# Optimization experiments

Hardware: AMD Instinct MI355X
Metric: run time of the kernel (lower is better)

The kernel has to match this reference:

```python
import jax, jax.numpy as jnp
import numpy as np

INV_148 = 1.0 / 1.48  # scaling to align grids with flat-top gaussian


def _trilinear_sample(grid, pts):
    # grid: [C, D, H, W]; pts: [N, 3] in (x,y,z)=(W,H,D) normalized coords, align_corners=True,
    # padding_mode='zeros' (out-of-bounds corners contribute 0). Returns [C, N].
    C, D, H, W = grid.shape
    fx = (pts[:, 0] + 1.0) * 0.5 * (W - 1)
    fy = (pts[:, 1] + 1.0) * 0.5 * (H - 1)
    fz = (pts[:, 2] + 1.0) * 0.5 * (D - 1)
    x0 = jnp.floor(fx).astype(jnp.int32)
    y0 = jnp.floor(fy).astype(jnp.int32)
    z0 = jnp.floor(fz).astype(jnp.int32)
    wx, wy, wz = fx - x0, fy - y0, fz - z0
    out = jnp.zeros((C, pts.shape[0]), dtype=grid.dtype)
    for dz in (0, 1):
        for dy in (0, 1):
            for dx in (0, 1):
                xi, yi, zi = x0 + dx, y0 + dy, z0 + dz
                w = (wx if dx else 1.0 - wx) * (wy if dy else 1.0 - wy) * (wz if dz else 1.0 - wz)
                valid = ((xi >= 0) & (xi < W) & (yi >= 0) & (yi < H) & (zi >= 0) & (zi < D))
                v = grid[:, jnp.clip(zi, 0, D - 1), jnp.clip(yi, 0, H - 1), jnp.clip(xi, 0, W - 1)]
                out = out + v * (w * valid)
    return out


def setup_inputs() -> dict:
    key = jax.random.key(0)
    ks = jax.random.split(key, 10)
    G, Fch, Dg, N, NPL, OUT = 32, 2, 64, 524288, 64, 1
    in_dim = G * Fch
    x = jax.random.uniform(ks[0], (N, 3), minval=-1.0, maxval=1.0, dtype=jnp.float32)
    grid_scales = jax.random.uniform(ks[1], (G, 3), minval=1.5, maxval=2.5, dtype=jnp.float32)
    grid_translations = jax.random.uniform(ks[2], (G, 3), minval=-1.0, maxval=1.0, dtype=jnp.float32) * (grid_scales - 1.0)
    feature_grids = jax.random.uniform(ks[3], (G, Fch, Dg, Dg, Dg), minval=-0.001, maxval=0.001, dtype=jnp.float32)
    W0 = jax.random.normal(ks[4], (NPL, in_dim), dtype=jnp.float32) * (1.0 / np.sqrt(in_dim))
    b0 = jnp.zeros((NPL,), dtype=jnp.float32)
    W1 = jax.random.normal(ks[5], (NPL, NPL), dtype=jnp.float32) * (1.0 / np.sqrt(NPL))
    b1 = jnp.zeros((NPL,), dtype=jnp.float32)
    W2 = jax.random.normal(ks[6], (OUT, NPL), dtype=jnp.float32) * (1.0 / np.sqrt(NPL))
    b2 = jnp.zeros((OUT,), dtype=jnp.float32)
    return {"x": x, "grid_scales": grid_scales, "grid_translations": grid_translations,
            "feature_grids": feature_grids, "W0": W0, "b0": b0, "W1": W1, "b1": b1, "W2": W2, "b2": b2}


def reference(x, grid_scales, grid_translations, feature_grids, W0, b0, W1, b1, W2, b2):
    G = feature_grids.shape[0]
    N = x.shape[0]
    # transform(): per-grid affine (diag scale + translation), then * 1/1.48 -> [G, N, 3]
    local = (x[None, :, :] * grid_scales[:, None, :] + grid_translations[:, None, :]) * INV_148
    # forward detaches grid coords before grid_sample
    local = jax.lax.stop_gradient(local)
    feats = jax.vmap(_trilinear_sample)(feature_grids, local)  # [G, F, N]
    h = feats.reshape(G * feats.shape[1], N).T  # [N, G*F]
    h = jax.nn.relu(h @ W0.T + b0)
    h = jax.nn.relu(h @ W1.T + b1)
    return h @ W2.T + b2  # [N, n_outputs]
```

## Files before the change

kernel.cpp:

```cpp
#include <hip/hip_runtime.h>
#include <hip/hip_fp16.h>

#define NG    32
#define DG    64
#define NPL   64
#define CPD2  16
#define NC2   4096
#define NCELL 512
#define NPAIR (NCELL * NG)
#define HPAD  16
#define BS    512
#define TV    4096
#define HS    68

#define SWZ(i) ((i) ^ (((i) >> 6) & 28))

typedef _Float16 half8 __attribute__((ext_vector_type(8)));
typedef float    floatx4 __attribute__((ext_vector_type(4)));

__device__ __forceinline__ int morton16(int cx, int cy, int cz) {
    int m = 0;
    #pragma unroll
    for (int b = 0; b < 4; ++b)
        m |= (((cx >> b) & 1) << (3 * b))
           | (((cy >> b) & 1) << (3 * b + 1))
           | (((cz >> b) & 1) << (3 * b + 2));
    return m;
}
__device__ __forceinline__ int cell_of(float px, float py, float pz) {
    int cx = min(max((int)((px + 1.0f) * (0.5f * CPD2)), 0), CPD2 - 1);
    int cy = min(max((int)((py + 1.0f) * (0.5f * CPD2)), 0), CPD2 - 1);
    int cz = min(max((int)((pz + 1.0f) * (0.5f * CPD2)), 0), CPD2 - 1);
    return morton16(cx, cy, cz);
}

__global__ __launch_bounds__(1024)
void classify_kernel(const float* __restrict__ scales,
                     const float* __restrict__ trans,
                     unsigned* __restrict__ pairs, int* __restrict__ counters)
{
    __shared__ int   sHead, sTail;
    __shared__ float sA[NG * 3], sB[NG * 3];
    const int tid  = threadIdx.x;
    const int lane = tid & 63;
    if (tid == 0) { sHead = 0; sTail = NPAIR; }
    if (tid < NG * 3) {
        const float k = (1.0f / 1.48f) * 31.5f;
        sA[tid] = scales[tid] * k;
        sB[tid] = trans[tid] * k + 31.5f;
    }
    __syncthreads();

    for (int p = tid; p < NPAIR; p += 1024) {
        int c = p >> 5, g = p & 31;
        int cx = (c & 1)        | (((c >> 3) & 1) << 1) | (((c >> 6) & 1) << 2);
        int cy = ((c >> 1) & 1) | (((c >> 4) & 1) << 1) | (((c >> 7) & 1) << 2);
        int cz = ((c >> 2) & 1) | (((c >> 5) & 1) << 1) | (((c >> 8) & 1) << 2);
        bool skip = false, fast = true;
        #pragma unroll
        for (int d = 0; d < 3; ++d) {
            float A = sA[3 * g + d], B = sB[3 * g + d];
            int  cc = (d == 0) ? cx : ((d == 1) ? cy : cz);
            float lo = fmaf((float)cc, 0.25f, -1.0f) - 1e-4f;
            float hi = lo + 0.25f + 2e-4f;
            float fmn = fmaf(lo, A, B);
            float fmx = fmaf(hi, A, B);
            skip = skip || (fmx <= -1.0f) || (fmn >= 64.0f);
            fast = fast && (fmn >= 0.0f) && (fmx <= 62.9f);
        }
        unsigned code = ((unsigned)c << 6) | ((unsigned)g << 1) | (fast ? 1u : 0u);

        unsigned long long mAct = __ballot(!skip);
        int cntA = __popcll(mAct);
        int bA = 0, bS = 0;
        if (lane == 0) {
            bA = atomicAdd(&sHead, cntA);
            bS = atomicAdd(&sTail, -(64 - cntA));
        }
        bA = __shfl(bA, 0); bS = __shfl(bS, 0);
        unsigned long long below = (1ull << lane) - 1ull;
        if (!skip) pairs[bA + __popcll(mAct & below)] = code;
        else       pairs[bS - 1 - __popcll(~mAct & below)] = code;
    }
    __syncthreads();
    if (tid == 0) counters[0] = sHead;
}

__global__ __launch_bounds__(256)
void pack_hist_kernel(const float* __restrict__ fg, uint4* __restrict__ pg,
                      int total4, int nPack,
                      const float* __restrict__ x, int N,
                      int* __restrict__ ghist)
{
    __shared__ int lh[NC2];
    if ((int)blockIdx.x < nPack) {
        int idx = blockIdx.x * 256 + threadIdx.x;
        if (idx >= total4) return;
        int g  = idx >> 16;
        int v4 = (idx & 65535) << 2;
        const float* base = fg + ((size_t)g << 19);
        float4 a = *(const float4*)(base + v4);
        float4 b = *(const float4*)(base + (1 << 18) + v4);
        uint4 o;
        __half2 h;
        h = __floats2half2_rn(a.x, b.x); o.x = *(unsigned*)&h;
        h = __floats2half2_rn(a.y, b.y); o.y = *(unsigned*)&h;
        h = __floats2half2_rn(a.z, b.z); o.z = *(unsigned*)&h;
        h = __floats2half2_rn(a.w, b.w); o.w = *(unsigned*)&h;
        pg[idx] = o;
    } else {
        int b = blockIdx.x - nPack;
        for (int i = threadIdx.x; i < NC2; i += 256) lh[i] = 0;
        __syncthreads();
        int base = b * 1024 + threadIdx.x;
        #pragma unroll
        for (int s = 0; s < 4; ++s) {
            int n = base + s * 256;
            if (n < N) atomicAdd(&lh[cell_of(x[3*n], x[3*n+1], x[3*n+2])], 1);
        }
        __syncthreads();
        for (int i = threadIdx.x; i < NC2; i += 256) {
            int c = lh[i];
            if (c) atomicAdd(&ghist[i * HPAD], c);
        }
    }
}

__global__ __launch_bounds__(1024)
void scan_kernel(const int* __restrict__ ghist, int* __restrict__ gcursor,
                 int* __restrict__ cellstart) {
    __shared__ int tsum[1024];
    int t = threadIdx.x;
    int v0 = ghist[(t * 4 + 0) * HPAD];
    int v1 = ghist[(t * 4 + 1) * HPAD];
    int v2 = ghist[(t * 4 + 2) * HPAD];
    int v3 = ghist[(t * 4 + 3) * HPAD];
    tsum[t] = v0 + v1 + v2 + v3;
    __syncthreads();
    #pragma unroll
    for (int off = 1; off < 1024; off <<= 1) {
        int u = (t >= off) ? tsum[t - off] : 0;
        __syncthreads();
        tsum[t] += u;
        __syncthreads();
    }
    int base = (t == 0) ? 0 : tsum[t - 1];
    gcursor[(t*4+0)*HPAD] = base; cellstart[t*4+0] = base; base += v0;
    gcursor[(t*4+1)*HPAD] = base; cellstart[t*4+1] = base; base += v1;
    gcursor[(t*4+2)*HPAD] = base; cellstart[t*4+2] = base; base += v2;
    gcursor[(t*4+3)*HPAD] = base; cellstart[t*4+3] = base;
    if (t == 1023) cellstart[NC2] = tsum[1023];
}

__global__ __launch_bounds__(BS)
void scatter_kernel(const float* __restrict__ x, int N,
                    int* __restrict__ gcursor, float4* __restrict__ sorted,
                    int* __restrict__ nidx) {
    __shared__ int cnt[NC2];
    __shared__ int base[NC2];
    int tid = threadIdx.x;
    for (int i = tid; i < NC2; i += BS) cnt[i] = 0;
    __syncthreads();
    int n = blockIdx.x * BS + tid;
    float px = 0.f, py = 0.f, pz = 0.f;
    int c = 0, r = 0;
    bool act = (n < N);
    if (act) {
        px = x[3*n]; py = x[3*n+1]; pz = x[3*n+2];
        c = cell_of(px, py, pz);
        r = atomicAdd(&cnt[c], 1);
    }
    __syncthreads();
    for (int i = tid; i < NC2; i += BS) {
        int cc = cnt[i];
        base[i] = cc ? atomicAdd(&gcursor[i * HPAD], cc) : 0;
    }
    __syncthreads();
    if (act) {
        int pos = base[c] + r;
        sorted[pos] = make_float4(px, py, pz, 0.0f);
        nidx[pos]   = n;
    }
}

__device__ __forceinline__ float2 h2_to_f2(unsigned u) {
    __half2 h = *reinterpret_cast<__half2*>(&u);
    return __half22float2(h);
}

template<bool FAST>
__device__ __forceinline__ unsigned sample_tile(
    const unsigned* __restrict__ tl,
    float px, float py, float pz,
    float A0, float A1, float A2, float B0, float B1, float B2,
    int ox, int oy, int oz)
{
    float fx = fmaf(px, A0, B0);
    float fy = fmaf(py, A1, B1);
    float fz = fmaf(pz, A2, B2);
    float flx = floorf(fx), fly = floorf(fy), flz = floorf(fz);
    int x0 = (int)flx, y0 = (int)fly, z0 = (int)flz;
    float wx = fx - flx, wy = fy - fly, wz = fz - flz;

    float wxa0, wxa1, wya0, wya1, wza0, wza1;
    int ix0, ix1, iy0, iy1, iz0, iz1;
    if (FAST) {
        wxa0 = 1.0f - wx; wxa1 = wx;
        wya0 = 1.0f - wy; wya1 = wy;
        wza0 = 1.0f - wz; wza1 = wz;
        ix0 = x0 - ox;            ix1 = ix0 + 1;
        iy0 = (y0 - oy) << 4;     iy1 = iy0 + 16;
        iz0 = (z0 - oz) << 8;     iz1 = iz0 + 256;
    } else {
        wxa0 = (x0 >= 0  && x0     < DG) ? (1.0f - wx) : 0.0f;
        wxa1 = (x0 >= -1 && x0 + 1 < DG) ? wx          : 0.0f;
        wya0 = (y0 >= 0  && y0     < DG) ? (1.0f - wy) : 0.0f;
        wya1 = (y0 >= -1 && y0 + 1 < DG) ? wy          : 0.0f;
        wza0 = (z0 >= 0  && z0     < DG) ? (1.0f - wz) : 0.0f;
        wza1 = (z0 >= -1 && z0 + 1 < DG) ? wz          : 0.0f;
        ix0 = min(max(x0     - ox, 0), 15);
        ix1 = min(max(x0 + 1 - ox, 0), 15);
        iy0 = (min(max(y0     - oy, 0), 15)) << 4;
        iy1 = (min(max(y0 + 1 - oy, 0), 15)) << 4;
        iz0 = (min(max(z0     - oz, 0), 15)) << 8;
        iz1 = (min(max(z0 + 1 - oz, 0), 15)) << 8;
    }
    const int m0 = (iz0 >> 6) & 28;
    const int m1 = (iz1 >> 6) & 28;

    float w00 = wya0 * wza0, w10 = wya1 * wza0;
    float w01 = wya0 * wza1, w11 = wya1 * wza1;

    float c0 = 0.0f, c1 = 0.0f;
    float2 v;
    v = h2_to_f2(tl[(iz0+iy0+ix0)^m0]); c0 = fmaf(wxa0*w00, v.x, c0); c1 = fmaf(wxa0*w00, v.y, c1);
    v = h2_to_f2(tl[(iz0+iy0+ix1)^m0]); c0 = fmaf(wxa1*w00, v.x, c0); c1 = fmaf(wxa1*w00, v.y, c1);
    v = h2_to_f2(tl[(iz0+iy1+ix0)^m0]); c0 = fmaf(wxa0*w10, v.x, c0); c1 = fmaf(wxa0*w10, v.y, c1);
    v = h2_to_f2(tl[(iz0+iy1+ix1)^m0]); c0 = fmaf(wxa1*w10, v.x, c0); c1 = fmaf(wxa1*w10, v.y, c1);
    v = h2_to_f2(tl[(iz1+iy0+ix0)^m1]); c0 = fmaf(wxa0*w01, v.x, c0); c1 = fmaf(wxa0*w01, v.y, c1);
    v = h2_to_f2(tl[(iz1+iy0+ix1)^m1]); c0 = fmaf(wxa1*w01, v.x, c0); c1 = fmaf(wxa1*w01, v.y, c1);
    v = h2_to_f2(tl[(iz1+iy1+ix0)^m1]); c0 = fmaf(wxa0*w11, v.x, c0); c1 = fmaf(wxa0*w11, v.y, c1);
    v = h2_to_f2(tl[(iz1+iy1+ix1)^m1]); c0 = fmaf(wxa1*w11, v.x, c0); c1 = fmaf(wxa1*w11, v.y, c1);

    __half2 hv = __floats2half2_rn(c0, c1);
    return *reinterpret_cast<unsigned*>(&hv);
}

__global__ __launch_bounds__(BS)
void gather2_kernel(const float4* __restrict__ sorted,
                    const int*   __restrict__ cs16,
                    const unsigned* __restrict__ pairs,
                    const int*   __restrict__ counters,
                    const float* __restrict__ scales,
                    const float* __restrict__ trans,
                    const unsigned* __restrict__ pg,
                    unsigned* __restrict__ fb, int N)
{
    __shared__ unsigned tile[TV];

    const int tid = threadIdx.x;
    const int nA  = counters[0];
    unsigned pr   = pairs[blockIdx.x];
    const int c   = pr >> 6;
    const int g   = (pr >> 1) & 31;
    const bool fastp = pr & 1;

    int s0 = cs16[c * 8];
    int e  = cs16[c * 8 + 8];

    if ((int)blockIdx.x >= nA) {
        for (int i = s0 + tid; i < e; i += BS) fb[(size_t)g * N + i] = 0u;
        return;
    }
    if (s0 >= e) return;

    int cx = (c & 1)        | (((c >> 3) & 1) << 1) | (((c >> 6) & 1) << 2);
    int cy = ((c >> 1) & 1) | (((c >> 4) & 1) << 1) | (((c >> 7) & 1) << 2);
    int cz = ((c >> 2) & 1) | (((c >> 5) & 1) << 1) | (((c >> 8) & 1) << 2);

    const float k = (1.0f / 1.48f) * 31.5f;
    float A0 = scales[3*g+0] * k, B0 = trans[3*g+0] * k + 31.5f;
    float A1 = scales[3*g+1] * k, B1 = trans[3*g+1] * k + 31.5f;
    float A2 = scales[3*g+2] * k, B2 = trans[3*g+2] * k + 31.5f;
    int ox = min(max((int)floorf(fmaf((float)cx * 0.25f - 1.0f, A0, B0)), 0), 48);
    int oy = min(max((int)floorf(fmaf((float)cy * 0.25f - 1.0f, A1, B1)), 0), 48);
    int oz = min(max((int)floorf(fmaf((float)cz * 0.25f - 1.0f, A2, B2)), 0), 48);

    float4 q0, q1, q2;
    int  i0 = s0 + tid, i1 = s0 + BS + tid, i2 = s0 + 2 * BS + tid;
    bool a0_ = (i0 < e), a1_ = (i1 < e), a2_ = (i2 < e);
    q0 = a0_ ? sorted[i0] : make_float4(0,0,0,0);
    q1 = a1_ ? sorted[i1] : make_float4(0,0,0,0);
    q2 = a2_ ? sorted[i2] : make_float4(0,0,0,0);

    const unsigned* gb = pg + ((size_t)g << 18);
    #pragma unroll
    for (int jj = 0; jj < 8; ++jj) {
        int v = tid + (jj << 9);
        tile[SWZ(v)] = gb[((oz + (v >> 8)) << 12) + ((oy + ((v >> 4) & 15)) << 6)
                          + ox + (v & 15)];
    }
    __syncthreads();

    unsigned* dst = fb + (size_t)g * N;
    if (fastp) {
        if (a0_) dst[i0] = sample_tile<true >(tile, q0.x,q0.y,q0.z, A0,A1,A2,B0,B1,B2, ox,oy,oz);
        if (a1_) dst[i1] = sample_tile<true >(tile, q1.x,q1.y,q1.z, A0,A1,A2,B0,B1,B2, ox,oy,oz);
        if (a2_) dst[i2] = sample_tile<true >(tile, q2.x,q2.y,q2.z, A0,A1,A2,B0,B1,B2, ox,oy,oz);
    } else {
        if (a0_) dst[i0] = sample_tile<false>(tile, q0.x,q0.y,q0.z, A0,A1,A2,B0,B1,B2, ox,oy,oz);
        if (a1_) dst[i1] = sample_tile<false>(tile, q1.x,q1.y,q1.z, A0,A1,A2,B0,B1,B2, ox,oy,oz);
        if (a2_) dst[i2] = sample_tile<false>(tile, q2.x,q2.y,q2.z, A0,A1,A2,B0,B1,B2, ox,oy,oz);
    }
}

#define MBS 256
__global__ __launch_bounds__(MBS)
void mlp_kernel(const unsigned* __restrict__ fb,
                const int* __restrict__ nidx,
                const float* __restrict__ W0, const float* __restrict__ b0,
                const float* __restrict__ W1, const float* __restrict__ b1,
                const float* __restrict__ W2, const float* __restrict__ b2,
                float* __restrict__ out, int N)
{
    __shared__ __align__(16) _Float16 sW0h[NPL * NPL];
    __shared__ __align__(16) _Float16 sW1h[NPL * NPL];
    __shared__ float sb0f[NPL], sb1f[NPL], sW2f[NPL];
    __shared__ __align__(16) _Float16 sH[4][NPL * HS];

    int tid = threadIdx.x;
    for (int i = tid; i < NPL * NPL; i += MBS) {
        sW0h[i] = (_Float16)W0[i];
        sW1h[i] = (_Float16)W1[i];
    }
    if (tid < NPL) { sb0f[tid] = b0[tid]; sb1f[tid] = b1[tid]; sW2f[tid] = W2[tid]; }
    __syncthreads();

    const int wave = tid >> 6;
    const int lane = tid & 63;
    const int l15  = lane & 15;
    const int kg   = lane >> 4;
    const long wbase = (long)blockIdx.x * MBS + wave * 64;
    if (wbase >= N) return;

    half8 B0f[4][2], B1f[4][2];
    float bias0[4], bias1[4], w2v[4];
    #pragma unroll
    for (int nt = 0; nt < 4; ++nt) {
        int ch = nt * 16 + l15;
        #pragma unroll
        for (int kh = 0; kh < 2; ++kh) {
            int k = kh * 32 + kg * 8;
            B0f[nt][kh] = *(const half8*)&sW0h[ch * NPL + k];
            B1f[nt][kh] = *(const half8*)&sW1h[ch * NPL + k];
        }
        bias0[nt] = sb0f[ch];
        bias1[nt] = sb1f[ch];
        w2v[nt]   = sW2f[ch];
    }

    _Float16* H = &sH[wave][0];

    floatx4 acc[4][4];
    #pragma unroll
    for (int mt = 0; mt < 4; ++mt) {
        long pt = wbase + mt * 16 + l15;
        if (pt > N - 1) pt = N - 1;
        const unsigned* p0 = fb + (size_t)(4 * kg) * N + pt;
        const unsigned* p1 = fb + (size_t)(16 + 4 * kg) * N + pt;
        uint4 t0 = make_uint4(p0[0], p0[N], p0[2*(size_t)N], p0[3*(size_t)N]);
        uint4 t1 = make_uint4(p1[0], p1[N], p1[2*(size_t)N], p1[3*(size_t)N]);
        half8 a0 = *reinterpret_cast<half8*>(&t0);
        half8 a1 = *reinterpret_cast<half8*>(&t1);
        #pragma unroll
        for (int nt = 0; nt < 4; ++nt) {
            floatx4 cc = {0.f, 0.f, 0.f, 0.f};
            cc = __builtin_amdgcn_mfma_f32_16x16x32_f16(a0, B0f[nt][0], cc, 0, 0, 0);
            cc = __builtin_amdgcn_mfma_f32_16x16x32_f16(a1, B0f[nt][1], cc, 0, 0, 0);
            acc[mt][nt] = cc;
        }
    }
    #pragma unroll
    for (int mt = 0; mt < 4; ++mt)
        #pragma unroll
        for (int nt = 0; nt < 4; ++nt) {
            int ch = nt * 16 + l15;
            #pragma unroll
            for (int r = 0; r < 4; ++r) {
                float v = fmaxf(acc[mt][nt][r] + bias0[nt], 0.0f);
                H[(mt * 16 + kg * 4 + r) * HS + ch] = (_Float16)v;
            }
        }

    floatx4 acc2[4][4];
    #pragma unroll
    for (int mt = 0; mt < 4; ++mt) {
        const _Float16* hp = &H[(mt * 16 + l15) * HS];
        half8 a0 = *(const half8*)&hp[kg * 8];
        half8 a1 = *(const half8*)&hp[32 + kg * 8];
        #pragma unroll
        for (int nt = 0; nt < 4; ++nt) {
            floatx4 cc = {0.f, 0.f, 0.f, 0.f};
            cc = __builtin_amdgcn_mfma_f32_16x16x32_f16(a0, B1f[nt][0], cc, 0, 0, 0);
            cc = __builtin_amdgcn_mfma_f32_16x16x32_f16(a1, B1f[nt][1], cc, 0, 0, 0);
            acc2[mt][nt] = cc;
        }
    }

    float p[4][4];
    #pragma unroll
    for (int mt = 0; mt < 4; ++mt)
        #pragma unroll
        for (int r = 0; r < 4; ++r) p[mt][r] = 0.0f;
    #pragma unroll
    for (int mt = 0; mt < 4; ++mt)
        #pragma unroll
        for (int nt = 0; nt < 4; ++nt)
            #pragma unroll
            for (int r = 0; r < 4; ++r) {
                float v = fmaxf(acc2[mt][nt][r] + bias1[nt], 0.0f);
                p[mt][r] = fmaf(v, w2v[nt], p[mt][r]);
            }
    #pragma unroll
    for (int mt = 0; mt < 4; ++mt)
        #pragma unroll
        for (int r = 0; r < 4; ++r) {
            float s = p[mt][r];
            s += __shfl_xor(s, 1);
            s += __shfl_xor(s, 2);
            s += __shfl_xor(s, 4);
            s += __shfl_xor(s, 8);
            p[mt][r] = s;
        }

    float* HF = (float*)H;
    float ob = b2[0];
    if (l15 == 0) {
        #pragma unroll
        for (int mt = 0; mt < 4; ++mt)
            #pragma unroll
            for (int r = 0; r < 4; ++r)
                HF[mt * 16 + kg * 4 + r] = p[mt][r] + ob;
    }
    long pos = wbase + lane;
    if (pos < N) out[nidx[pos]] = HF[lane];
}

__global__ void pack_only_kernel(const float* __restrict__ fg,
                                 uint4* __restrict__ pg, int total4) {
    int idx = blockIdx.x * blockDim.x + threadIdx.x;
    if (idx >= total4) return;
    int g  = idx >> 16;
    int v4 = (idx & 65535) << 2;
    const float* base = fg + ((size_t)g << 19);
    float4 a = *(const float4*)(base + v4);
    float4 b = *(const float4*)(base + (1 << 18) + v4);
    uint4 o;
    __half2 h;
    h = __floats2half2_rn(a.x, b.x); o.x = *(unsigned*)&h;
    h = __floats2half2_rn(a.y, b.y); o.y = *(unsigned*)&h;
    h = __floats2half2_rn(a.z, b.z); o.z = *(unsigned*)&h;
    h = __floats2half2_rn(a.w, b.w); o.w = *(unsigned*)&h;
    pg[idx] = o;
}

__global__ __launch_bounds__(256)
void fused_fallback_kernel(const float* __restrict__ x,
                           const float* __restrict__ scales,
                           const float* __restrict__ trans,
                           const __half2* __restrict__ pg,
                           const float* __restrict__ W0, const float* __restrict__ b0,
                           const float* __restrict__ W1, const float* __restrict__ b1,
                           const float* __restrict__ W2, const float* __restrict__ b2,
                           float* __restrict__ out, int N)
{
    __shared__ float sW0[NPL*NPL], sW1[NPL*NPL], sW2[NPL], sb0[NPL], sb1[NPL];
    __shared__ float sA[NG*3], sB[NG*3];
    const int tid = threadIdx.x;
    for (int i = tid; i < NPL*NPL; i += 256) { sW0[i] = W0[i]; sW1[i] = W1[i]; }
    if (tid < NPL) { sW2[tid] = W2[tid]; sb0[tid] = b0[tid]; sb1[tid] = b1[tid]; }
    if (tid < NG*3) {
        const float k = (1.0f / 1.48f) * 31.5f;
        sA[tid] = scales[tid] * k;
        sB[tid] = trans[tid] * k + 31.5f;
    }
    __syncthreads();
    int n = blockIdx.x * 256 + tid;
    if (n >= N) return;
    float px = x[3*n], py = x[3*n+1], pz = x[3*n+2];
    float feat[2*NG];
    #pragma unroll
    for (int g = 0; g < NG; ++g) {
        float fx = fmaf(px, sA[3*g+0], sB[3*g+0]);
        float fy = fmaf(py, sA[3*g+1], sB[3*g+1]);
        float fz = fmaf(pz, sA[3*g+2], sB[3*g+2]);
        float c0 = 0.f, c1 = 0.f;
        if (fx > -1.f && fx < 64.f && fy > -1.f && fy < 64.f && fz > -1.f && fz < 64.f) {
            float flx = floorf(fx), fly = floorf(fy), flz = floorf(fz);
            int x0 = (int)flx, y0 = (int)fly, z0 = (int)flz;
            float wx = fx-flx, wy = fy-fly, wz = fz-flz;
            float wxa[2], wya[2], wza[2]; int xia[2], yia[2], zia[2];
            wxa[0] = (x0 >= 0  && x0   < DG) ? (1.f-wx) : 0.f;
            wxa[1] = (x0 >= -1 && x0+1 < DG) ? wx : 0.f;
            wya[0] = (y0 >= 0  && y0   < DG) ? (1.f-wy) : 0.f;
            wya[1] = (y0 >= -1 && y0+1 < DG) ? wy : 0.f;
            wza[0] = (z0 >= 0  && z0   < DG) ? (1.f-wz) : 0.f;
            wza[1] = (z0 >= -1 && z0+1 < DG) ? wz : 0.f;
            xia[0] = min(max(x0,0),DG-1); xia[1] = min(max(x0+1,0),DG-1);
            yia[0] = min(max(y0,0),DG-1); yia[1] = min(max(y0+1,0),DG-1);
            zia[0] = min(max(z0,0),DG-1); zia[1] = min(max(z0+1,0),DG-1);
            #pragma unroll
            for (int dz = 0; dz < 2; ++dz)
                #pragma unroll
                for (int dy = 0; dy < 2; ++dy) {
                    int rowoff = (zia[dz] << 12) + (yia[dy] << 6);
                    float wyz = wya[dy] * wza[dz];
                    #pragma unroll
                    for (int dx = 0; dx < 2; ++dx) {
                        float w = wxa[dx] * wyz;
                        float2 vf = __half22float2(pg[(g << 18) + rowoff + xia[dx]]);
                        c0 = fmaf(w, vf.x, c0); c1 = fmaf(w, vf.y, c1);
                    }
                }
        }
        feat[2*g] = c0; feat[2*g+1] = c1;
    }
    float h1[NPL];
    #pragma unroll
    for (int j = 0; j < NPL; j += 2) {
        float a0=0.f,a1=0.f,a2=0.f,a3=0.f;
        const float* r0 = &sW0[j*NPL]; const float* r1 = &sW0[(j+1)*NPL];
        #pragma unroll
        for (int k = 0; k < NPL; k += 2) {
            a0 = fmaf(feat[k],r0[k],a0); a1 = fmaf(feat[k+1],r0[k+1],a1);
            a2 = fmaf(feat[k],r1[k],a2); a3 = fmaf(feat[k+1],r1[k+1],a3);
        }
        h1[j] = fmaxf((a0+a1)+sb0[j],0.f); h1[j+1] = fmaxf((a2+a3)+sb0[j+1],0.f);
    }
    #pragma unroll
    for (int j = 0; j < NPL; j += 2) {
        float a0=0.f,a1=0.f,a2=0.f,a3=0.f;
        const float* r0 = &sW1[j*NPL]; const float* r1 = &sW1[(j+1)*NPL];
        #pragma unroll
        for (int k = 0; k < NPL; k += 2) {
            a0 = fmaf(h1[k],r0[k],a0); a1 = fmaf(h1[k+1],r0[k+1],a1);
            a2 = fmaf(h1[k],r1[k],a2); a3 = fmaf(h1[k+1],r1[k+1],a3);
        }
        feat[j] = fmaxf((a0+a1)+sb1[j],0.f); feat[j+1] = fmaxf((a2+a3)+sb1[j+1],0.f);
    }
    float a0 = 0.f, a1 = 0.f;
    #pragma unroll
    for (int k = 0; k < NPL; k += 2) { a0 = fmaf(feat[k],sW2[k],a0); a1 = fmaf(feat[k+1],sW2[k+1],a1); }
    out[n] = (a0+a1) + b2[0];
}

extern "C" void kernel_launch(void* const* d_in, const int* in_sizes, int n_in,
                              void* d_out, int out_size, void* d_ws, size_t ws_size,
                              hipStream_t stream) {
    const float* x  = (const float*)d_in[0];
    const float* gs = (const float*)d_in[1];
    const float* gt = (const float*)d_in[2];
    const float* fg = (const float*)d_in[3];
    const float* W0 = (const float*)d_in[4];
    const float* b0 = (const float*)d_in[5];
    const float* W1 = (const float*)d_in[6];
    const float* b1 = (const float*)d_in[7];
    const float* W2 = (const float*)d_in[8];
    const float* b2 = (const float*)d_in[9];
    float* out = (float*)d_out;

    const int N = out_size;

    const size_t pg_bytes    = (size_t)NG * (1 << 18) * 4;
    const size_t fb_bytes    = (size_t)N * NG * 4;
    const size_t sort_bytes  = (size_t)N * sizeof(float4);
    const size_t nidx_bytes  = (size_t)N * sizeof(int);
    const size_t cs_bytes    = ((NC2 + 1 + 15) & ~15) * sizeof(int);
    const size_t hist_bytes  = (size_t)NC2 * HPAD * sizeof(int);
    const size_t pairs_bytes = (size_t)NPAIR * 4;
    const size_t ctr_bytes   = 64;
    const size_t need_full   = pg_bytes + fb_bytes + sort_bytes + nidx_bytes
                             + cs_bytes + 2 * hist_bytes + pairs_bytes + ctr_bytes;

    if (ws_size >= need_full) {
        char* w = (char*)d_ws;
        unsigned* pg        = (unsigned*)w;  w += pg_bytes;
        unsigned* fb        = (unsigned*)w;  w += fb_bytes;
        float4*   sorted    = (float4*)w;    w += sort_bytes;
        int*      nidx      = (int*)w;       w += nidx_bytes;
        int*      cellstart = (int*)w;       w += cs_bytes;
        int*      ghist     = (int*)w;       w += hist_bytes;
        int*      gcur      = (int*)w;       w += hist_bytes;
        unsigned* pairs     = (unsigned*)w;  w += pairs_bytes;
        int*      counters  = (int*)w;

        int total4 = NG << 16;
        int nPack  = total4 / 256;
        int nHist  = (N + 1023) / 1024;
        int nblkS  = (N + BS - 1) / BS;

        classify_kernel<<<1, 1024, 0, stream>>>(gs, gt, pairs, counters);
        hipMemsetAsync(ghist, 0, hist_bytes, stream);
        pack_hist_kernel<<<nPack + nHist, 256, 0, stream>>>(
            fg, (uint4*)pg, total4, nPack, x, N, ghist);
        scan_kernel<<<1, 1024, 0, stream>>>(ghist, gcur, cellstart);
        scatter_kernel<<<nblkS, BS, 0, stream>>>(x, N, gcur, sorted, nidx);
        gather2_kernel<<<NPAIR, BS, 0, stream>>>(
            sorted, cellstart, pairs, counters, gs, gt, pg, fb, N);
        mlp_kernel<<<(N + MBS - 1) / MBS, MBS, 0, stream>>>(
            fb, nidx, W0, b0, W1, b1, W2, b2, out, N);
    } else if (ws_size >= pg_bytes) {
        unsigned* pg = (unsigned*)d_ws;
        int total4 = NG << 16;
        pack_only_kernel<<<(total4 + 255) / 256, 256, 0, stream>>>(fg, (uint4*)pg, total4);
        fused_fallback_kernel<<<(N + 255) / 256, 256, 0, stream>>>(
            x, gs, gt, (const __half2*)pg, W0, b0, W1, b1, W2, b2, out, N);
    } else {
        fused_fallback_kernel<<<(N + 255) / 256, 256, 0, stream>>>(
            x, gs, gt, (const __half2*)fg, W0, b0, W1, b1, W2, b2, out, N);
    }
}
```

Before: 186.8 us.

## Fuse classify/pack prelude and histogram-scan-scatter into a cooperative sort kernel

Merges the classify and memset work into the grid-packing kernel as an extra block, and replaces the separate histogram, scan and scatter launches with one cooperative kernel that uses grid-wide syncs. The MLP kernel now loads its weights straight from global memory into registers instead of staging them in shared memory, and gets an occupancy hint. This is meant to cut kernel launch count and inter-kernel gaps, at the cost of grid.sync barriers, a serial single-block classify/zeroing path, and more redundant global weight loads per wave.

Measured after the change: 401.0 us. +114.6%, slower.

```diff
diff --git a/kernel.cpp b/kernel.cpp
--- a/kernel.cpp
+++ b/kernel.cpp
@@ -1,5 +1,8 @@
 #include <hip/hip_runtime.h>
 #include <hip/hip_fp16.h>
+#include <hip/hip_cooperative_groups.h>
+
+namespace cg = cooperative_groups;
 
 #define NG    32
 #define DG    64
@@ -34,67 +37,20 @@
     return morton16(cx, cy, cz);
 }
 
-__global__ __launch_bounds__(1024)
-void classify_kernel(const float* __restrict__ scales,
-                     const float* __restrict__ trans,
-                     unsigned* __restrict__ pairs, int* __restrict__ counters)
+__global__ __launch_bounds__(256)
+void prelude_kernel(const float* __restrict__ fg, uint4* __restrict__ pg,
+                    int total4, int nPack,
+                    const float* __restrict__ scales,
+                    const float* __restrict__ trans,
+                    unsigned* __restrict__ pairs, int* __restrict__ counters,
+                    int* __restrict__ ghist)
 {
     __shared__ int   sHead, sTail;
     __shared__ float sA[NG * 3], sB[NG * 3];
-    const int tid  = threadIdx.x;
-    const int lane = tid & 63;
-    if (tid == 0) { sHead = 0; sTail = NPAIR; }
-    if (tid < NG * 3) {
-        const float k = (1.0f / 1.48f) * 31.5f;
-        sA[tid] = scales[tid] * k;
-        sB[tid] = trans[tid] * k + 31.5f;
-    }
-    __syncthreads();
-
-    for (int p = tid; p < NPAIR; p += 1024) {
-        int c = p >> 5, g = p & 31;
-        int cx = (c & 1)        | (((c >> 3) & 1) << 1) | (((c >> 6) & 1) << 2);
-        int cy = ((c >> 1) & 1) | (((c >> 4) & 1) << 1) | (((c >> 7) & 1) << 2);
-        int cz = ((c >> 2) & 1) | (((c >> 5) & 1) << 1) | (((c >> 8) & 1) << 2);
-        bool skip = false, fast = true;
-        #pragma unroll
-        for (int d = 0; d < 3; ++d) {
-            float A = sA[3 * g + d], B = sB[3 * g + d];
-            int  cc = (d == 0) ? cx : ((d == 1) ? cy : cz);
-            float lo = fmaf((float)cc, 0.25f, -1.0f) - 1e-4f;
-            float hi = lo + 0.25f + 2e-4f;
-            float fmn = fmaf(lo, A, B);
-            float fmx = fmaf(hi, A, B);
-            skip = skip || (fmx <= -1.0f) || (fmn >= 64.0f);
-            fast = fast && (fmn >= 0.0f) && (fmx <= 62.9f);
-        }
-        unsigned code = ((unsigned)c << 6) | ((unsigned)g << 1) | (fast ? 1u : 0u);
-
-        unsigned long long mAct = __ballot(!skip);
-        int cntA = __popcll(mAct);
-        int bA = 0, bS = 0;
-        if (lane == 0) {
-            bA = atomicAdd(&sHead, cntA);
-            bS = atomicAdd(&sTail, -(64 - cntA));
-        }
-        bA = __shfl(bA, 0); bS = __shfl(bS, 0);
-        unsigned long long below = (1ull << lane) - 1ull;
-        if (!skip) pairs[bA + __popcll(mAct & below)] = code;
-        else       pairs[bS - 1 - __popcll(~mAct & below)] = code;
-    }
-    __syncthreads();
-    if (tid == 0) counters[0] = sHead;
-}
-
-__global__ __launch_bounds__(256)
-void pack_hist_kernel(const float* __restrict__ fg, uint4* __restrict__ pg,
-                      int total4, int nPack,
-                      const float* __restrict__ x, int N,
-                      int* __restrict__ ghist)
-{
-    __shared__ int lh[NC2];
+    const int tid = threadIdx.x;
+
     if ((int)blockIdx.x < nPack) {
-        int idx = blockIdx.x * 256 + threadIdx.x;
+        int idx = blockIdx.x * 256 + tid;
         if (idx >= total4) return;
         int g  = idx >> 16;
         int v4 = (idx & 65535) << 2;
@@ -108,21 +64,133 @@
         h = __floats2half2_rn(a.z, b.z); o.z = *(unsigned*)&h;
         h = __floats2half2_rn(a.w, b.w); o.w = *(unsigned*)&h;
         pg[idx] = o;
-    } else {
-        int b = blockIdx.x - nPack;
-        for (int i = threadIdx.x; i < NC2; i += 256) lh[i] = 0;
+        return;
+    }
+
+    const int lane = tid & 63;
+    if (tid == 0) { sHead = 0; sTail = NPAIR; }
+    if (tid < NG * 3) {
+        const float k = (1.0f / 1.48f) * 31.5f;
+        sA[tid] = scales[tid] * k;
+        sB[tid] = trans[tid] * k + 31.5f;
+    }
+    for (int i = tid; i < NC2 * HPAD; i += 256) ghist[i] = 0;
+    __syncthreads();
+
+    for (int p = tid; p < NPAIR; p += 256) {
+        int c = p >> 5, g = p & 31;
+        int cx = (c & 1)        | (((c >> 3) & 1) << 1) | (((c >> 6) & 1) << 2);
+        int cy = ((c >> 1) & 1) | (((c >> 4) & 1) << 1) | (((c >> 7) & 1) << 2);
+        int cz = ((c >> 2) & 1) | (((c >> 5) & 1) << 1) | (((c >> 8) & 1) << 2);
+        bool skip = false, fast = true;
+        #pragma unroll
+        for (int d = 0; d < 3; ++d) {
+            float A = sA[3 * g + d], B = sB[3 * g + d];
+            int  cc = (d == 0) ? cx : ((d == 1) ? cy : cz);
+            float lo = fmaf((float)cc, 0.25f, -1.0f) - 1e-4f;
+            float hi = lo + 0.25f + 2e-4f;
+            float fmn = fmaf(lo, A, B);
+            float fmx = fmaf(hi, A, B);
+            skip = skip || (fmx <= -1.0f) || (fmn >= 64.0f);
+            fast = fast && (fmn >= 0.0f) && (fmx <= 62.9f);
+        }
+        unsigned code = ((unsigned)c << 6) | ((unsigned)g << 1) | (fast ? 1u : 0u);
+
+        unsigned long long mAct = __ballot(!skip);
+        int cntA = __popcll(mAct);
+        int bA = 0, bS = 0;
+        if (lane == 0) {
+            bA = atomicAdd(&sHead, cntA);
+            bS = atomicAdd(&sTail, -(64 - cntA));
+        }
+        bA = __shfl(bA, 0); bS = __shfl(bS, 0);
+        unsigned long long below = (1ull << lane) - 1ull;
+        if (!skip) pairs[bA + __popcll(mAct & below)] = code;
+        else       pairs[bS - 1 - __popcll(~mAct & below)] = code;
+    }
+    __syncthreads();
+    if (tid == 0) counters[0] = sHead;
+}
+
+__global__ __launch_bounds__(512)
+void sort_coop_kernel(const float* __restrict__ x, int N,
+                      int* __restrict__ ghist, int* __restrict__ gcursor,
+                      int* __restrict__ cellstart,
+                      float4* __restrict__ sorted, int* __restrict__ nidx)
+{
+    cg::grid_group grid = cg::this_grid();
+    __shared__ int lh[NC2];
+    __shared__ int lbase[NC2];
+    __shared__ int tsum[512];
+
+    const int tid = threadIdx.x;
+    for (int i = tid; i < NC2; i += 512) lh[i] = 0;
+    __syncthreads();
+
+    int n = blockIdx.x * 512 + tid;
+    bool act = (n < N);
+    float px = 0.f, py = 0.f, pz = 0.f;
+    int c = 0, r = 0;
+    if (act) {
+        px = x[3*n]; py = x[3*n+1]; pz = x[3*n+2];
+        c = cell_of(px, py, pz);
+        r = atomicAdd(&lh[c], 1);
+    }
+    __syncthreads();
+    for (int i = tid; i < NC2; i += 512) {
+        int cc = lh[i];
+        if (cc) atomicAdd(&ghist[i * HPAD], cc);
+    }
+
+    grid.sync();
+
+    if (blockIdx.x == 0) {
+        int v[8]; int s = 0;
+        #pragma unroll
+        for (int j = 0; j < 8; ++j) { v[j] = ghist[(tid * 8 + j) * HPAD]; s += v[j]; }
+        tsum[tid] = s;
         __syncthreads();
-        int base = b * 1024 + threadIdx.x;
-        #pragma unroll
-        for (int s = 0; s < 4; ++s) {
-            int n = base + s * 256;
-            if (n < N) atomicAdd(&lh[cell_of(x[3*n], x[3*n+1], x[3*n+2])], 1);
-        }
-        __syncthreads();
-        for (int i = threadIdx.x; i < NC2; i += 256) {
-            int c = lh[i];
-            if (c) atomicAdd(&ghist[i * HPAD], c);
-        }
+        for (int off = 1; off < 512; off <<= 1) {
+            int u = (tid >= off) ? tsum[tid - off] : 0;
+            __syncthreads();
+            tsum[tid] += u;
+            __syncthreads();
+        }
+        int base = (tid == 0) ? 0 : tsum[tid - 1];
+        #pragma unroll
+        for (int j = 0; j < 8; ++j) {
+            gcursor[(tid * 8 + j) * HPAD] = base;
+            cellstart[tid * 8 + j] = base;
+            base += v[j];
+        }
+        if (tid == 511) cellstart[NC2] = tsum[511];
+    }
+
+    grid.sync();
+
+    for (int i = tid; i < NC2; i += 512) {
+        int cc = lh[i];
+        lbase[i] = cc ? atomicAdd(&gcursor[i * HPAD], cc) : 0;
+    }
+    __syncthreads();
+    if (act) {
+        int pos = lbase[c] + r;
+        sorted[pos] = make_float4(px, py, pz, 0.0f);
+        nidx[pos]   = n;
+    }
+}
+
+__global__ __launch_bounds__(BS)
+void hist_kernel(const float* __restrict__ x, int N, int* __restrict__ ghist) {
+    __shared__ int lh[NC2];
+    for (int i = threadIdx.x; i < NC2; i += BS) lh[i] = 0;
+    __syncthreads();
+    int n = blockIdx.x * BS + threadIdx.x;
+    if (n < N) atomicAdd(&lh[cell_of(x[3*n], x[3*n+1], x[3*n+2])], 1);
+    __syncthreads();
+    for (int i = threadIdx.x; i < NC2; i += BS) {
+        int c = lh[i];
+        if (c) atomicAdd(&ghist[i * HPAD], c);
     }
 }
 
@@ -315,7 +383,7 @@
 }
 
 #define MBS 256
-__global__ __launch_bounds__(MBS)
+__global__ __launch_bounds__(MBS, 4)
 void mlp_kernel(const unsigned* __restrict__ fb,
                 const int* __restrict__ nidx,
                 const float* __restrict__ W0, const float* __restrict__ b0,
@@ -323,19 +391,9 @@
                 const float* __restrict__ W2, const float* __restrict__ b2,
                 float* __restrict__ out, int N)
 {
-    __shared__ __align__(16) _Float16 sW0h[NPL * NPL];
-    __shared__ __align__(16) _Float16 sW1h[NPL * NPL];
-    __shared__ float sb0f[NPL], sb1f[NPL], sW2f[NPL];
     __shared__ __align__(16) _Float16 sH[4][NPL * HS];
 
-    int tid = threadIdx.x;
-    for (int i = tid; i < NPL * NPL; i += MBS) {
-        sW0h[i] = (_Float16)W0[i];
-        sW1h[i] = (_Float16)W1[i];
-    }
-    if (tid < NPL) { sb0f[tid] = b0[tid]; sb1f[tid] = b1[tid]; sW2f[tid] = W2[tid]; }
-    __syncthreads();
-
+    const int tid  = threadIdx.x;
     const int wave = tid >> 6;
     const int lane = tid & 63;
     const int l15  = lane & 15;
@@ -351,12 +409,17 @@
         #pragma unroll
         for (int kh = 0; kh < 2; ++kh) {
             int k = kh * 32 + kg * 8;
-            B0f[nt][kh] = *(const half8*)&sW0h[ch * NPL + k];
-            B1f[nt][kh] = *(const half8*)&sW1h[ch * NPL + k];
-        }
-        bias0[nt] = sb0f[ch];
-        bias1[nt] = sb1f[ch];
-        w2v[nt]   = sW2f[ch];
+            const float* w0p = &W0[ch * NPL + k];
+            const float* w1p = &W1[ch * NPL + k];
+            half8 h0, h1;
+            #pragma unroll
+            for (int i = 0; i < 8; ++i) { h0[i] = (_Float16)w0p[i]; h1[i] = (_Float16)w1p[i]; }
+            B0f[nt][kh] = h0;
+            B1f[nt][kh] = h1;
+        }
+        bias0[nt] = b0[ch];
+        bias1[nt] = b1[ch];
+        w2v[nt]   = W2[ch];
     }
 
     _Float16* H = &sH[wave][0];
@@ -596,17 +659,33 @@
 
         int total4 = NG << 16;
         int nPack  = total4 / 256;
-        int nHist  = (N + 1023) / 1024;
-        int nblkS  = (N + BS - 1) / BS;
-
-        classify_kernel<<<1, 1024, 0, stream>>>(gs, gt, pairs, counters);
-        hipMemsetAsync(ghist, 0, hist_bytes, stream);
-        pack_hist_kernel<<<nPack + nHist, 256, 0, stream>>>(
-            fg, (uint4*)pg, total4, nPack, x, N, ghist);
-        scan_kernel<<<1, 1024, 0, stream>>>(ghist, gcur, cellstart);
-        scatter_kernel<<<nblkS, BS, 0, stream>>>(x, N, gcur, sorted, nidx);
+        int nblkC  = (N + 511) / 512;
+
+        prelude_kernel<<<nPack + 1, 256, 0, stream>>>(
+            fg, (uint4*)pg, total4, nPack, gs, gt, pairs, counters, ghist);
+
+        bool coop_ok = false;
+        if (nblkC <= 1024) {
+            const float* x_ = x; int N_ = N;
+            int* gh_ = ghist; int* gc_ = gcur; int* cs_ = cellstart;
+            float4* so_ = sorted; int* ni_ = nidx;
+            void* args[] = { (void*)&x_, (void*)&N_, (void*)&gh_, (void*)&gc_,
+                             (void*)&cs_, (void*)&so_, (void*)&ni_ };
+            hipError_t e = hipLaunchCooperativeKernel(
+                (const void*)sort_coop_kernel, dim3(nblkC), dim3(512),
+                args, 0, stream);
+            coop_ok = (e == hipSuccess);
+        }
+        if (!coop_ok) {
+            int nblkS = (N + BS - 1) / BS;
+            hist_kernel<<<nblkS, BS, 0, stream>>>(x, N, ghist);
+            scan_kernel<<<1, 1024, 0, stream>>>(ghist, gcur, cellstart);
+            scatter_kernel<<<nblkS, BS, 0, stream>>>(x, N, gcur, sorted, nidx);
+        }
+
         gather2_kernel<<<NPAIR, BS, 0, stream>>>(
             sorted, cellstart, pairs, counters, gs, gt, pg, fb, N);
+
         mlp_kernel<<<(N + MBS - 1) / MBS, MBS, 0, stream>>>(
             fb, nidx, W0, b0, W1, b1, W2, b2, out, N);
     } else if (ws_size >= pg_bytes) {
```

## Convert grids to fp16 inside gather tile load and merge classify into histogram kernel

Applied to the files above, without the earlier changes.

Drops the separate pre-pass that packed the fp32 feature grids into an interleaved fp16 buffer. The gather kernel now reads the two fp32 channel planes directly and converts them to half2 while filling its shared tile. The classify work also moves into an extra block of the histogram kernel, removing one launch. This avoids writing and re-reading a 32 MB packed buffer, but each gather block now does two strided fp32 loads per tile element instead of one 32-bit load, and overlapping tiles re-read more bytes. The fallback path also changed: it now reads the fp32 grids directly instead of the old fp16 path, which reinterpreted the fp32 grids as half2 (a latent bug).

Result: slower. 219.7 us (+17.6%).

```diff
diff --git a/kernel.cpp b/kernel.cpp
--- a/kernel.cpp
+++ b/kernel.cpp
@@ -34,16 +34,37 @@
     return morton16(cx, cy, cz);
 }
 
-__global__ __launch_bounds__(1024)
-void classify_kernel(const float* __restrict__ scales,
+__global__ __launch_bounds__(256)
+void sortprep_kernel(const float* __restrict__ x, int N, int nHist,
+                     int* __restrict__ ghist,
+                     const float* __restrict__ scales,
                      const float* __restrict__ trans,
                      unsigned* __restrict__ pairs, int* __restrict__ counters)
 {
-    __shared__ int   sHead, sTail;
+    __shared__ int lh[NC2];
+    const int tid = threadIdx.x;
+    const int bid = blockIdx.x;
+
+    if (bid < nHist) {
+        for (int i = tid; i < NC2; i += 256) lh[i] = 0;
+        __syncthreads();
+        int base = bid * 1024 + tid;
+        #pragma unroll
+        for (int s = 0; s < 4; ++s) {
+            int n = base + s * 256;
+            if (n < N) atomicAdd(&lh[cell_of(x[3*n], x[3*n+1], x[3*n+2])], 1);
+        }
+        __syncthreads();
+        for (int i = tid; i < NC2; i += 256) {
+            int c = lh[i];
+            if (c) atomicAdd(&ghist[i * HPAD], c);
+        }
+        return;
+    }
+
     __shared__ float sA[NG * 3], sB[NG * 3];
-    const int tid  = threadIdx.x;
     const int lane = tid & 63;
-    if (tid == 0) { sHead = 0; sTail = NPAIR; }
+    if (tid == 0) { lh[0] = 0; lh[1] = NPAIR; }
     if (tid < NG * 3) {
         const float k = (1.0f / 1.48f) * 31.5f;
         sA[tid] = scales[tid] * k;
@@ -51,7 +72,7 @@
     }
     __syncthreads();
 
-    for (int p = tid; p < NPAIR; p += 1024) {
+    for (int p = tid; p < NPAIR; p += 256) {
         int c = p >> 5, g = p & 31;
         int cx = (c & 1)        | (((c >> 3) & 1) << 1) | (((c >> 6) & 1) << 2);
         int cy = ((c >> 1) & 1) | (((c >> 4) & 1) << 1) | (((c >> 7) & 1) << 2);
@@ -74,8 +95,8 @@
         int cntA = __popcll(mAct);
         int bA = 0, bS = 0;
         if (lane == 0) {
-            bA = atomicAdd(&sHead, cntA);
-            bS = atomicAdd(&sTail, -(64 - cntA));
+            bA = atomicAdd(&lh[0], cntA);
+            bS = atomicAdd(&lh[1], -(64 - cntA));
         }
         bA = __shfl(bA, 0); bS = __shfl(bS, 0);
         unsigned long long below = (1ull << lane) - 1ull;
@@ -83,47 +104,7 @@
         else       pairs[bS - 1 - __popcll(~mAct & below)] = code;
     }
     __syncthreads();
-    if (tid == 0) counters[0] = sHead;
-}
-
-__global__ __launch_bounds__(256)
-void pack_hist_kernel(const float* __restrict__ fg, uint4* __restrict__ pg,
-                      int total4, int nPack,
-                      const float* __restrict__ x, int N,
-                      int* __restrict__ ghist)
-{
-    __shared__ int lh[NC2];
-    if ((int)blockIdx.x < nPack) {
-        int idx = blockIdx.x * 256 + threadIdx.x;
-        if (idx >= total4) return;
-        int g  = idx >> 16;
-        int v4 = (idx & 65535) << 2;
-        const float* base = fg + ((size_t)g << 19);
-        float4 a = *(const float4*)(base + v4);
-        float4 b = *(const float4*)(base + (1 << 18) + v4);
-        uint4 o;
-        __half2 h;
-        h = __floats2half2_rn(a.x, b.x); o.x = *(unsigned*)&h;
-        h = __floats2half2_rn(a.y, b.y); o.y = *(unsigned*)&h;
-        h = __floats2half2_rn(a.z, b.z); o.z = *(unsigned*)&h;
-        h = __floats2half2_rn(a.w, b.w); o.w = *(unsigned*)&h;
-        pg[idx] = o;
-    } else {
-        int b = blockIdx.x - nPack;
-        for (int i = threadIdx.x; i < NC2; i += 256) lh[i] = 0;
-        __syncthreads();
-        int base = b * 1024 + threadIdx.x;
-        #pragma unroll
-        for (int s = 0; s < 4; ++s) {
-            int n = base + s * 256;
-            if (n < N) atomicAdd(&lh[cell_of(x[3*n], x[3*n+1], x[3*n+2])], 1);
-        }
-        __syncthreads();
-        for (int i = threadIdx.x; i < NC2; i += 256) {
-            int c = lh[i];
-            if (c) atomicAdd(&ghist[i * HPAD], c);
-        }
-    }
+    if (tid == 0) counters[0] = lh[0];
 }
 
 __global__ __launch_bounds__(1024)
@@ -247,13 +228,13 @@
 }
 
 __global__ __launch_bounds__(BS)
-void gather2_kernel(const float4* __restrict__ sorted,
+void gather3_kernel(const float4* __restrict__ sorted,
                     const int*   __restrict__ cs16,
                     const unsigned* __restrict__ pairs,
                     const int*   __restrict__ counters,
                     const float* __restrict__ scales,
                     const float* __restrict__ trans,
-                    const unsigned* __restrict__ pg,
+                    const float* __restrict__ fg,
                     unsigned* __restrict__ fb, int N)
 {
     __shared__ unsigned tile[TV];
@@ -293,12 +274,15 @@
     q1 = a1_ ? sorted[i1] : make_float4(0,0,0,0);
     q2 = a2_ ? sorted[i2] : make_float4(0,0,0,0);
 
-    const unsigned* gb = pg + ((size_t)g << 18);
+    const float* gb0 = fg + ((size_t)g << 19);
+    const float* gb1 = gb0 + (1 << 18);
     #pragma unroll
     for (int jj = 0; jj < 8; ++jj) {
-        int v = tid + (jj << 9);
-        tile[SWZ(v)] = gb[((oz + (v >> 8)) << 12) + ((oy + ((v >> 4) & 15)) << 6)
-                          + ox + (v & 15)];
+        int v  = tid + (jj << 9);
+        int gi = ((oz + (v >> 8)) << 12) + ((oy + ((v >> 4) & 15)) << 6)
+                 + ox + (v & 15);
+        __half2 h = __floats2half2_rn(gb0[gi], gb1[gi]);
+        tile[SWZ(v)] = *reinterpret_cast<unsigned*>(&h);
     }
     __syncthreads();
 
@@ -446,29 +430,12 @@
     if (pos < N) out[nidx[pos]] = HF[lane];
 }
 
-__global__ void pack_only_kernel(const float* __restrict__ fg,
-                                 uint4* __restrict__ pg, int total4) {
-    int idx = blockIdx.x * blockDim.x + threadIdx.x;
-    if (idx >= total4) return;
-    int g  = idx >> 16;
-    int v4 = (idx & 65535) << 2;
-    const float* base = fg + ((size_t)g << 19);
-    float4 a = *(const float4*)(base + v4);
-    float4 b = *(const float4*)(base + (1 << 18) + v4);
-    uint4 o;
-    __half2 h;
-    h = __floats2half2_rn(a.x, b.x); o.x = *(unsigned*)&h;
-    h = __floats2half2_rn(a.y, b.y); o.y = *(unsigned*)&h;
-    h = __floats2half2_rn(a.z, b.z); o.z = *(unsigned*)&h;
-    h = __floats2half2_rn(a.w, b.w); o.w = *(unsigned*)&h;
-    pg[idx] = o;
-}
-
+template<bool GRIDS_F32>
 __global__ __launch_bounds__(256)
 void fused_fallback_kernel(const float* __restrict__ x,
                            const float* __restrict__ scales,
                            const float* __restrict__ trans,
-                           const __half2* __restrict__ pg,
+                           const void* __restrict__ grids,
                            const float* __restrict__ W0, const float* __restrict__ b0,
                            const float* __restrict__ W1, const float* __restrict__ b1,
                            const float* __restrict__ W2, const float* __restrict__ b2,
@@ -518,8 +485,15 @@
                     #pragma unroll
                     for (int dx = 0; dx < 2; ++dx) {
                         float w = wxa[dx] * wyz;
-                        float2 vf = __half22float2(pg[(g << 18) + rowoff + xia[dx]]);
-                        c0 = fmaf(w, vf.x, c0); c1 = fmaf(w, vf.y, c1);
+                        if (GRIDS_F32) {
+                            const float* fr = (const float*)grids + ((size_t)g << 19);
+                            c0 = fmaf(w, fr[rowoff + xia[dx]], c0);
+                            c1 = fmaf(w, fr[(1 << 18) + rowoff + xia[dx]], c1);
+                        } else {
+                            const __half2* pgp = (const __half2*)grids;
+                            float2 vf = __half22float2(pgp[(g << 18) + rowoff + xia[dx]]);
+                            c0 = fmaf(w, vf.x, c0); c1 = fmaf(w, vf.y, c1);
+                        }
                     }
                 }
         }
@@ -571,7 +545,6 @@
 
     const int N = out_size;
 
-    const size_t pg_bytes    = (size_t)NG * (1 << 18) * 4;
     const size_t fb_bytes    = (size_t)N * NG * 4;
     const size_t sort_bytes  = (size_t)N * sizeof(float4);
     const size_t nidx_bytes  = (size_t)N * sizeof(int);
@@ -579,12 +552,11 @@
     const size_t hist_bytes  = (size_t)NC2 * HPAD * sizeof(int);
     const size_t pairs_bytes = (size_t)NPAIR * 4;
     const size_t ctr_bytes   = 64;
-    const size_t need_full   = pg_bytes + fb_bytes + sort_bytes + nidx_bytes
+    const size_t need_full   = fb_bytes + sort_bytes + nidx_bytes
                              + cs_bytes + 2 * hist_bytes + pairs_bytes + ctr_bytes;
 
     if (ws_size >= need_full) {
         char* w = (char*)d_ws;
-        unsigned* pg        = (unsigned*)w;  w += pg_bytes;
         unsigned* fb        = (unsigned*)w;  w += fb_bytes;
         float4*   sorted    = (float4*)w;    w += sort_bytes;
         int*      nidx      = (int*)w;       w += nidx_bytes;
@@ -594,29 +566,20 @@
         unsigned* pairs     = (unsigned*)w;  w += pairs_bytes;
         int*      counters  = (int*)w;
 
-        int total4 = NG << 16;
-        int nPack  = total4 / 256;
-        int nHist  = (N + 1023) / 1024;
-        int nblkS  = (N + BS - 1) / BS;
-
-        classify_kernel<<<1, 1024, 0, stream>>>(gs, gt, pairs, counters);
+        int nHist = (N + 1023) / 1024;
+        int nblkS = (N + BS - 1) / BS;
+
         hipMemsetAsync(ghist, 0, hist_bytes, stream);
-        pack_hist_kernel<<<nPack + nHist, 256, 0, stream>>>(
-            fg, (uint4*)pg, total4, nPack, x, N, ghist);
+        sortprep_kernel<<<nHist + 1, 256, 0, stream>>>(
+            x, N, nHist, ghist, gs, gt, pairs, counters);
         scan_kernel<<<1, 1024, 0, stream>>>(ghist, gcur, cellstart);
         scatter_kernel<<<nblkS, BS, 0, stream>>>(x, N, gcur, sorted, nidx);
-        gather2_kernel<<<NPAIR, BS, 0, stream>>>(
-            sorted, cellstart, pairs, counters, gs, gt, pg, fb, N);
+        gather3_kernel<<<NPAIR, BS, 0, stream>>>(
+            sorted, cellstart, pairs, counters, gs, gt, fg, fb, N);
         mlp_kernel<<<(N + MBS - 1) / MBS, MBS, 0, stream>>>(
             fb, nidx, W0, b0, W1, b1, W2, b2, out, N);
-    } else if (ws_size >= pg_bytes) {
-        unsigned* pg = (unsigned*)d_ws;
-        int total4 = NG << 16;
-        pack_only_kernel<<<(total4 + 255) / 256, 256, 0, stream>>>(fg, (uint4*)pg, total4);
-        fused_fallback_kernel<<<(N + 255) / 256, 256, 0, stream>>>(
-            x, gs, gt, (const __half2*)pg, W0, b0, W1, b1, W2, b2, out, N);
     } else {
-        fused_fallback_kernel<<<(N + 255) / 256, 256, 0, stream>>>(
-            x, gs, gt, (const __half2*)fg, W0, b0, W1, b1, W2, b2, out, N);
-    }
-}
+        fused_fallback_kernel<true><<<(N + 255) / 256, 256, 0, stream>>>(
+            x, gs, gt, fg, W0, b0, W1, b1, W2, b2, out, N);
+    }
+}
```
